# Optimization experiments

Hardware: AMD Instinct MI355X
Metric: run time of the kernel (lower is better)

## Reference

```python
import jax, jax.numpy as jnp
import numpy as np

B, C, L = 4, 256, 4096
H = 8
DK = C // H


def setup_inputs() -> dict:
    key = jax.random.key(0)
    kx, kq, kk, kv, kl = jax.random.split(key, 5)
    scale = 1.0 / np.sqrt(C)
    return {
        "x": jax.random.normal(kx, (B, C, L), dtype=jnp.float32),
        "Wq": jax.random.normal(kq, (C, C), dtype=jnp.float32) * scale,
        "Wk": jax.random.normal(kk, (C, C), dtype=jnp.float32) * scale,
        "Wv": jax.random.normal(kv, (C, C), dtype=jnp.float32) * scale,
        "Wl": jax.random.normal(kl, (C, C), dtype=jnp.float32) * scale,
    }


def reference(x, Wq, Wk, Wv, Wl):
    # Conv1d with kernel_size=1, no bias == channel-mixing matmul per position.
    def proj(W, t):  # W: [C_out, C_in], t: [B, C_in, L] -> [B, L, H, DK]
        y = jnp.einsum('oc,bcl->blo', W, t)
        return y.reshape(B, L, H, DK)

    q = proj(Wq, x)  # [B, L, H, DK]
    k = proj(Wk, x)
    v = proj(Wv, x)

    # scores: [B, H, L, L]
    scores = jnp.einsum('bqhd,bkhd->bhqk', q, k) / jnp.sqrt(jnp.float32(DK))
    p_attn = jax.nn.softmax(scores, axis=-1)
    # attention output with post-ReLU: [B, L, H, DK] -> [B, L, C]
    out = jax.nn.relu(jnp.einsum('bhqk,bkhd->bqhd', p_attn, v)).reshape(B, L, C)
    # last_conv: [B, C_out, L]
    return jnp.einsum('oc,blc->bol', Wl, out)
```

## Files before the change

kernel.cpp:

```cpp
#include <hip/hip_runtime.h>

#define L_DIM 4096
#define C_DIM 256
#define B_DIM 4
#define NH 8
#define DK 32

#define QSCALE 0.25507694f

typedef __bf16 bf16x8 __attribute__((ext_vector_type(8)));
typedef float  f32x4  __attribute__((ext_vector_type(4)));
typedef float  f32x8  __attribute__((ext_vector_type(8)));
typedef float  f32x16 __attribute__((ext_vector_type(16)));

static __device__ __forceinline__ unsigned pk_bf16(float lo, float hi) {
    unsigned a = __builtin_bit_cast(unsigned, lo) + 0x8000u;
    unsigned b = __builtin_bit_cast(unsigned, hi) + 0x8000u;
    return __builtin_amdgcn_perm(b, a, 0x07060302u);
}

__global__ __launch_bounds__(256) void transpose_x_kernel(
    const float* __restrict__ x, __bf16* __restrict__ xt)
{
    const int t  = threadIdx.x;
    const int l0 = blockIdx.x * 64;
    const int c0 = blockIdx.y * 64;
    const int b  = blockIdx.z;

    __shared__ __attribute__((aligned(16))) float T[64][65];

    {
        const int r  = t >> 2;
        const int lc = (t & 3) * 16;
        const float* xp = x + ((size_t)b * C_DIM + c0 + r) * L_DIM + l0 + lc;
        #pragma unroll
        for (int k = 0; k < 4; ++k)
            *(f32x4*)&T[r][lc + k * 4] = *(const f32x4*)(xp + k * 4);
    }
    __syncthreads();
    {
        const int l  = t >> 2;
        const int cc = (t & 3) * 16;
        unsigned u[8];
        #pragma unroll
        for (int i = 0; i < 8; ++i)
            u[i] = pk_bf16(T[cc + 2 * i][l], T[cc + 2 * i + 1][l]);
        __bf16* op = xt + ((size_t)b * L_DIM + l0 + l) * C_DIM + c0 + cc;
        *(uint4*)op       = make_uint4(u[0], u[1], u[2], u[3]);
        *(uint4*)(op + 8) = make_uint4(u[4], u[5], u[6], u[7]);
    }
}

__global__ __launch_bounds__(256) void proj_mfma_kernel(
    const __bf16* __restrict__ xt, const float* __restrict__ Wq,
    const float* __restrict__ Wk, const float* __restrict__ Wv,
    __bf16* __restrict__ Qb, __bf16* __restrict__ Kb, __bf16* __restrict__ Vb)
{
    const int t    = threadIdx.x;
    const int wave = t >> 6;
    const int lane = t & 63;
    const int n32  = lane & 31;
    const int hl   = lane >> 5;
    const int l0   = blockIdx.x * 128;
    const int ob   = blockIdx.y & 1;
    const int p    = blockIdx.y >> 1;
    const int b    = blockIdx.z;
    const float* W = (p == 0) ? Wq : ((p == 1) ? Wk : Wv);
    const float sc = (p == 0) ? QSCALE : 1.0f;

    __shared__ __attribute__((aligned(16))) __bf16 Wt[128][72];
    __shared__ __attribute__((aligned(16))) __bf16 Xs[128][72];

    const int wo  = t >> 1, wcc = (t & 1) * 32;
    const int xl  = t >> 1, xcc = (t & 1) * 32;
    const float*  wg = W + (size_t)(ob * 128 + wo) * C_DIM + wcc;
    const __bf16* xg = xt + ((size_t)b * L_DIM + l0 + xl) * C_DIM + xcc;

    const int moff = (wave & 1) * 64;
    const int noff = (wave >> 1) * 64;

    f32x16 acc[2][2];
    #pragma unroll
    for (int i = 0; i < 2; ++i)
        #pragma unroll
        for (int j = 0; j < 2; ++j)
            #pragma unroll
            for (int r = 0; r < 16; ++r) acc[i][j][r] = 0.f;

    unsigned wpk[16];
    bf16x8   xpr[4];
    #pragma unroll
    for (int k = 0; k < 8; ++k) {
        f32x4 wv = *(const f32x4*)(wg + k * 4);
        wpk[k * 2]     = pk_bf16(wv[0] * sc, wv[1] * sc);
        wpk[k * 2 + 1] = pk_bf16(wv[2] * sc, wv[3] * sc);
    }
    #pragma unroll
    for (int g = 0; g < 4; ++g) xpr[g] = *(const bf16x8*)(xg + g * 8);

    for (int bk = 0; bk < 4; ++bk) {
        __syncthreads();
        #pragma unroll
        for (int g = 0; g < 4; ++g) {
            *(uint4*)&Wt[wo][wcc + g * 8] =
                make_uint4(wpk[g*4], wpk[g*4+1], wpk[g*4+2], wpk[g*4+3]);
            *(bf16x8*)&Xs[xl][xcc + g * 8] = xpr[g];
        }
        if (bk < 3) {
            #pragma unroll
            for (int k = 0; k < 8; ++k) {
                f32x4 wv = *(const f32x4*)(wg + (bk + 1) * 64 + k * 4);
                wpk[k * 2]     = pk_bf16(wv[0] * sc, wv[1] * sc);
                wpk[k * 2 + 1] = pk_bf16(wv[2] * sc, wv[3] * sc);
            }
            #pragma unroll
            for (int g = 0; g < 4; ++g)
                xpr[g] = *(const bf16x8*)(xg + (bk + 1) * 64 + g * 8);
        }
        __syncthreads();

        #pragma unroll
        for (int ks = 0; ks < 4; ++ks) {
            bf16x8 a0 = *(const bf16x8*)&Wt[moff + n32     ][ks * 16 + hl * 8];
            bf16x8 a1 = *(const bf16x8*)&Wt[moff + 32 + n32][ks * 16 + hl * 8];
            bf16x8 b0 = *(const bf16x8*)&Xs[noff + n32     ][ks * 16 + hl * 8];
            bf16x8 b1 = *(const bf16x8*)&Xs[noff + 32 + n32][ks * 16 + hl * 8];
            acc[0][0] = __builtin_amdgcn_mfma_f32_32x32x16_bf16(a0, b0, acc[0][0], 0, 0, 0);
            acc[0][1] = __builtin_amdgcn_mfma_f32_32x32x16_bf16(a0, b1, acc[0][1], 0, 0, 0);
            acc[1][0] = __builtin_amdgcn_mfma_f32_32x32x16_bf16(a1, b0, acc[1][0], 0, 0, 0);
            acc[1][1] = __builtin_amdgcn_mfma_f32_32x32x16_bf16(a1, b1, acc[1][1], 0, 0, 0);
        }
    }

    #pragma unroll
    for (int mt = 0; mt < 2; ++mt) {
        const int o32 = ob * 128 + moff + mt * 32;
        const int h   = o32 >> 5;
        const int bh  = b * NH + h;
        #pragma unroll
        for (int nt = 0; nt < 2; ++nt) {
            const int l = l0 + noff + nt * 32 + n32;
            if (p < 2) {
                __bf16* out = ((p == 0) ? Qb : Kb) + ((size_t)bh * L_DIM + l) * DK;
                #pragma unroll
                for (int g = 0; g < 4; ++g) {
                    unsigned u0 = pk_bf16(acc[mt][nt][g*4],     acc[mt][nt][g*4+1]);
                    unsigned u1 = pk_bf16(acc[mt][nt][g*4+2],   acc[mt][nt][g*4+3]);
                    *(uint2*)(out + 4 * hl + 8 * g) = make_uint2(u0, u1);
                }
            } else {
                #pragma unroll
                for (int r = 0; r < 16; ++r) {
                    const int dk = (r & 3) + 4 * hl + 8 * (r >> 2);
                    Vb[((size_t)bh * DK + dk) * L_DIM + l] = (__bf16)acc[mt][nt][r];
                }
            }
        }
    }
}

__global__ __launch_bounds__(256) void attn_kernel(
    const __bf16* __restrict__ Q, const __bf16* __restrict__ K,
    const __bf16* __restrict__ V, __bf16* __restrict__ Op0,
    __bf16* __restrict__ Op1, float* __restrict__ Ls)
{
    const int tid   = threadIdx.x;
    const int wave  = tid >> 6;
    const int lane  = tid & 63;
    const int n32   = lane & 31;
    const int hl    = lane >> 5;
    const int h     = blockIdx.y;
    const int b     = blockIdx.z >> 1;
    const int khalf = blockIdx.z & 1;
    const int bh    = b * NH + h;
    const int q0    = blockIdx.x * 256 + wave * 64;
    const int kt0   = khalf * 32;

    __shared__ __attribute__((aligned(16))) __bf16 Ks[2][64][40];
    __shared__ __attribute__((aligned(16))) __bf16 Vs[2][32][72];

    bf16x8 qf[2][2];
    #pragma unroll
    for (int qt = 0; qt < 2; ++qt) {
        const __bf16* qp = Q + ((size_t)bh * L_DIM + q0 + qt * 32 + n32) * DK;
        qf[qt][0] = *(const bf16x8*)(qp + hl * 8);
        qf[qt][1] = *(const bf16x8*)(qp + 16 + hl * 8);
    }

    f32x16 oacc[2], lacc[2];
    #pragma unroll
    for (int qt = 0; qt < 2; ++qt)
        #pragma unroll
        for (int r = 0; r < 16; ++r) { oacc[qt][r] = 0.f; lacc[qt][r] = 0.f; }

    const f32x16 z16 = {};

    bf16x8 ones;
    #pragma unroll
    for (int j = 0; j < 8; ++j) ones[j] = (__bf16)1.0f;

    const __bf16* kg = K + (size_t)bh * L_DIM * DK + (tid >> 2) * DK + (tid & 3) * 8;
    const __bf16* vg = V + ((size_t)bh * DK + (tid >> 3)) * L_DIM + (tid & 7) * 8;
    const int kr = tid >> 2, kc = (tid & 3) * 8;
    const int va = tid & 7;
    const int vr = tid >> 3, vc = (va >> 1) * 16 + (va & 1) * 4;

    bf16x8 kreg = *(const bf16x8*)(kg + (size_t)kt0 * 64 * DK);
    bf16x8 vreg = *(const bf16x8*)(vg + kt0 * 64);
    *(bf16x8*)&Ks[0][kr][kc] = kreg;
    {
        union { bf16x8 v; uint2 u2[2]; } vv; vv.v = vreg;
        *(uint2*)&Vs[0][vr][vc]     = vv.u2[0];
        *(uint2*)&Vs[0][vr][vc + 8] = vv.u2[1];
    }
    kreg = *(const bf16x8*)(kg + (size_t)(kt0 + 1) * 64 * DK);
    vreg = *(const bf16x8*)(vg + (kt0 + 1) * 64);

    #pragma unroll 2
    for (int kt = 0; kt < 32; ++kt) {
        const int cur = kt & 1;
        __syncthreads();

        bf16x8 kf[2][2];
        kf[0][0] = *(const bf16x8*)&Ks[cur][n32     ][hl * 8];
        kf[0][1] = *(const bf16x8*)&Ks[cur][n32     ][16 + hl * 8];
        kf[1][0] = *(const bf16x8*)&Ks[cur][32 + n32][hl * 8];
        kf[1][1] = *(const bf16x8*)&Ks[cur][32 + n32][16 + hl * 8];
        bf16x8 vf[4];
        vf[0] = *(const bf16x8*)&Vs[cur][n32][     hl * 8];
        vf[1] = *(const bf16x8*)&Vs[cur][n32][16 + hl * 8];
        vf[2] = *(const bf16x8*)&Vs[cur][n32][32 + hl * 8];
        vf[3] = *(const bf16x8*)&Vs[cur][n32][48 + hl * 8];

        if (kt < 31) {
            *(bf16x8*)&Ks[cur ^ 1][kr][kc] = kreg;
            union { bf16x8 v; uint2 u2[2]; } vv; vv.v = vreg;
            *(uint2*)&Vs[cur ^ 1][vr][vc]     = vv.u2[0];
            *(uint2*)&Vs[cur ^ 1][vr][vc + 8] = vv.u2[1];
            const int nkt = kt0 + ((kt + 2) & 31);
            kreg = *(const bf16x8*)(kg + (size_t)nkt * 64 * DK);
            vreg = *(const bf16x8*)(vg + nkt * 64);
        }

        #pragma unroll
        for (int mt = 0; mt < 2; ++mt) {
            #pragma unroll
            for (int qt = 0; qt < 2; ++qt) {
                f32x16 s = __builtin_amdgcn_mfma_f32_32x32x16_bf16(
                    kf[mt][0], qf[qt][0], z16, 0, 0, 0);
                s = __builtin_amdgcn_mfma_f32_32x32x16_bf16(
                    kf[mt][1], qf[qt][1], s, 0, 0, 0);

                f32x8 e0, e1;
                #pragma unroll
                for (int r = 0; r < 8; ++r) {
                    e0[r] = __builtin_amdgcn_exp2f(s[r]);
                    e1[r] = __builtin_amdgcn_exp2f(s[8 + r]);
                }
                bf16x8 p0 = __builtin_convertvector(e0, bf16x8);
                bf16x8 p1 = __builtin_convertvector(e1, bf16x8);

                oacc[qt] = __builtin_amdgcn_mfma_f32_32x32x16_bf16(
                    vf[mt * 2],     p0, oacc[qt], 0, 0, 0);
                lacc[qt] = __builtin_amdgcn_mfma_f32_32x32x16_bf16(
                    ones,           p0, lacc[qt], 0, 0, 0);
                oacc[qt] = __builtin_amdgcn_mfma_f32_32x32x16_bf16(
                    vf[mt * 2 + 1], p1, oacc[qt], 0, 0, 0);
                lacc[qt] = __builtin_amdgcn_mfma_f32_32x32x16_bf16(
                    ones,           p1, lacc[qt], 0, 0, 0);
            }
        }
    }

    __bf16* Op = khalf ? Op1 : Op0;
    #pragma unroll
    for (int qt = 0; qt < 2; ++qt) {
        const int l = q0 + qt * 32 + n32;
        __bf16* ap = Op + ((size_t)b * L_DIM + l) * C_DIM + h * 32 + 4 * hl;
        #pragma unroll
        for (int g = 0; g < 4; ++g) {
            *(uint2*)(ap + 8 * g) = make_uint2(
                pk_bf16(oacc[qt][g*4],     oacc[qt][g*4+1]),
                pk_bf16(oacc[qt][g*4+2],   oacc[qt][g*4+3]));
        }
        Ls[((size_t)khalf * B_DIM * NH + bh) * L_DIM + l] = lacc[qt][0];
    }
}

__global__ __launch_bounds__(256) void final_mfma_kernel(
    const __bf16* __restrict__ Op0, const __bf16* __restrict__ Op1,
    const float* __restrict__ Ls, const float* __restrict__ Wl,
    float* __restrict__ y)
{
    const int t    = threadIdx.x;
    const int wave = t >> 6;
    const int lane = t & 63;
    const int n32  = lane & 31;
    const int hl   = lane >> 5;
    const int l0   = blockIdx.x * 64;
    const int ob   = blockIdx.y;
    const int b    = blockIdx.z;

    __shared__ __attribute__((aligned(16))) __bf16 Wt[128][72];
    __shared__ __attribute__((aligned(16))) __bf16 Xs[64][72];

    const int wo  = t >> 1, wcc = (t & 1) * 32;
    const int xl  = t >> 2, xcc = (t & 3) * 16;
    const float* wg = Wl + (size_t)(ob * 128 + wo) * C_DIM + wcc;
    const size_t obase = ((size_t)b * L_DIM + l0 + xl) * C_DIM + xcc;

    float inv[4];
    {
        const int lidx = l0 + xl;
        #pragma unroll
        for (int bk = 0; bk < 4; ++bk) {
            const int hh = (bk * 64 + xcc) >> 5;
            const float l1 = Ls[((size_t)0 * B_DIM * NH + b * NH + hh) * L_DIM + lidx];
            const float l2 = Ls[((size_t)1 * B_DIM * NH + b * NH + hh) * L_DIM + lidx];
            inv[bk] = __builtin_amdgcn_rcpf(l1 + l2);
        }
    }

    const int moff = (wave & 1) * 64;
    const int noff = (wave >> 1) * 32;

    f32x16 acc[2];
    #pragma unroll
    for (int i = 0; i < 2; ++i)
        #pragma unroll
        for (int r = 0; r < 16; ++r) acc[i][r] = 0.f;

    unsigned wpk[16];
    bf16x8   o1r, o2r;
    #pragma unroll
    for (int k = 0; k < 8; ++k) {
        f32x4 wv = *(const f32x4*)(wg + k * 4);
        wpk[k * 2]     = pk_bf16(wv[0], wv[1]);
        wpk[k * 2 + 1] = pk_bf16(wv[2], wv[3]);
    }
    o1r = *(const bf16x8*)(Op0 + obase);
    o2r = *(const bf16x8*)(Op1 + obase);
    bf16x8 o1r2 = *(const bf16x8*)(Op0 + obase + 8);
    bf16x8 o2r2 = *(const bf16x8*)(Op1 + obase + 8);

    for (int bk = 0; bk < 4; ++bk) {
        __syncthreads();
        #pragma unroll
        for (int g = 0; g < 4; ++g)
            *(uint4*)&Wt[wo][wcc + g * 8] =
                make_uint4(wpk[g*4], wpk[g*4+1], wpk[g*4+2], wpk[g*4+3]);
        {
            unsigned u[4];
            #pragma unroll
            for (int i = 0; i < 4; ++i) {
                float v0 = ((float)o1r[2*i]   + (float)o2r[2*i]  ) * inv[bk];
                float v1 = ((float)o1r[2*i+1] + (float)o2r[2*i+1]) * inv[bk];
                v0 = v0 > 0.f ? v0 : 0.f;
                v1 = v1 > 0.f ? v1 : 0.f;
                u[i] = pk_bf16(v0, v1);
            }
            *(uint4*)&Xs[xl][xcc] = make_uint4(u[0], u[1], u[2], u[3]);
            #pragma unroll
            for (int i = 0; i < 4; ++i) {
                float v0 = ((float)o1r2[2*i]   + (float)o2r2[2*i]  ) * inv[bk];
                float v1 = ((float)o1r2[2*i+1] + (float)o2r2[2*i+1]) * inv[bk];
                v0 = v0 > 0.f ? v0 : 0.f;
                v1 = v1 > 0.f ? v1 : 0.f;
                u[i] = pk_bf16(v0, v1);
            }
            *(uint4*)&Xs[xl][xcc + 8] = make_uint4(u[0], u[1], u[2], u[3]);
        }
        if (bk < 3) {
            #pragma unroll
            for (int k = 0; k < 8; ++k) {
                f32x4 wv = *(const f32x4*)(wg + (bk + 1) * 64 + k * 4);
                wpk[k * 2]     = pk_bf16(wv[0], wv[1]);
                wpk[k * 2 + 1] = pk_bf16(wv[2], wv[3]);
            }
            o1r  = *(const bf16x8*)(Op0 + obase + (bk + 1) * 64);
            o2r  = *(const bf16x8*)(Op1 + obase + (bk + 1) * 64);
            o1r2 = *(const bf16x8*)(Op0 + obase + (bk + 1) * 64 + 8);
            o2r2 = *(const bf16x8*)(Op1 + obase + (bk + 1) * 64 + 8);
        }
        __syncthreads();

        #pragma unroll
        for (int ks = 0; ks < 4; ++ks) {
            bf16x8 a0 = *(const bf16x8*)&Wt[moff + n32     ][ks * 16 + hl * 8];
            bf16x8 a1 = *(const bf16x8*)&Wt[moff + 32 + n32][ks * 16 + hl * 8];
            bf16x8 b0 = *(const bf16x8*)&Xs[noff + n32     ][ks * 16 + hl * 8];
            acc[0] = __builtin_amdgcn_mfma_f32_32x32x16_bf16(a0, b0, acc[0], 0, 0, 0);
            acc[1] = __builtin_amdgcn_mfma_f32_32x32x16_bf16(a1, b0, acc[1], 0, 0, 0);
        }
    }

    #pragma unroll
    for (int mt = 0; mt < 2; ++mt) {
        #pragma unroll
        for (int r = 0; r < 16; ++r) {
            const int o = ob * 128 + moff + mt * 32 + (r & 3) + 4 * hl + 8 * (r >> 2);
            y[((size_t)b * C_DIM + o) * L_DIM + l0 + noff + n32] = acc[mt][r];
        }
    }
}

extern "C" void kernel_launch(void* const* d_in, const int* in_sizes, int n_in,
                              void* d_out, int out_size, void* d_ws, size_t ws_size,
                              hipStream_t stream)
{
    const float* x  = (const float*)d_in[0];
    const float* Wq = (const float*)d_in[1];
    const float* Wk = (const float*)d_in[2];
    const float* Wv = (const float*)d_in[3];
    const float* Wl = (const float*)d_in[4];
    float* y = (float*)d_out;

    const size_t n = (size_t)B_DIM * NH * L_DIM * DK;
    __bf16* Qb  = (__bf16*)d_ws;
    __bf16* Kb  = Qb + n;
    __bf16* Vb  = Kb + n;
    __bf16* Xt  = Vb + n;
    __bf16* Op0 = Xt;
    __bf16* Op1 = Xt + n;
    float*  Ls  = (float*)(Op1 + n);

    transpose_x_kernel<<<dim3(L_DIM/64, C_DIM/64, B_DIM), 256, 0, stream>>>(x, Xt);
    proj_mfma_kernel<<<dim3(L_DIM/128, 6, B_DIM), 256, 0, stream>>>(
        Xt, Wq, Wk, Wv, Qb, Kb, Vb);
    attn_kernel<<<dim3(L_DIM/256, NH, B_DIM * 2), 256, 0, stream>>>(
        Qb, Kb, Vb, Op0, Op1, Ls);
    final_mfma_kernel<<<dim3(L_DIM/64, 2, B_DIM), 256, 0, stream>>>(
        Op0, Op1, Ls, Wl, y);
}
```

Measured before the change: 211.2 us.

## Double attention K/V tile to 128 keys and interleave LDS fragment loads

The attention kernel now stages 128 keys per iteration instead of 64, so it runs 16 loop iterations with half as many barriers. Each thread loads two 16-byte chunks of K and V per stage. K/V fragments are read from LDS inside the mt loop right before they are used, not all up front, which lowers register pressure. s_setprio raises wave priority around the MFMA/exp section. LDS use roughly doubles, which could cut occupancy, and the new V shared-memory permutation must still match the MFMA operand layout.

Result: no change. 211.2 us (-0.0%).

```diff
diff --git a/kernel.cpp b/kernel.cpp
--- a/kernel.cpp
+++ b/kernel.cpp
@@ -165,19 +165,18 @@
     __bf16* __restrict__ Op1, float* __restrict__ Ls)
 {
     const int tid   = threadIdx.x;
-    const int wave  = tid >> 6;
     const int lane  = tid & 63;
     const int n32   = lane & 31;
     const int hl    = lane >> 5;
+    const int wave  = tid >> 6;
     const int h     = blockIdx.y;
     const int b     = blockIdx.z >> 1;
     const int khalf = blockIdx.z & 1;
     const int bh    = b * NH + h;
     const int q0    = blockIdx.x * 256 + wave * 64;
-    const int kt0   = khalf * 32;
-
-    __shared__ __attribute__((aligned(16))) __bf16 Ks[2][64][40];
-    __shared__ __attribute__((aligned(16))) __bf16 Vs[2][32][72];
+
+    __shared__ __attribute__((aligned(16))) __bf16 Ks[2][128][40];
+    __shared__ __attribute__((aligned(16))) __bf16 Vs[2][32][136];
 
     bf16x8 qf[2][2];
     #pragma unroll
@@ -199,57 +198,67 @@
     #pragma unroll
     for (int j = 0; j < 8; ++j) ones[j] = (__bf16)1.0f;
 
-    const __bf16* kg = K + (size_t)bh * L_DIM * DK + (tid >> 2) * DK + (tid & 3) * 8;
-    const __bf16* vg = V + ((size_t)bh * DK + (tid >> 3)) * L_DIM + (tid & 7) * 8;
-    const int kr = tid >> 2, kc = (tid & 3) * 8;
-    const int va = tid & 7;
-    const int vr = tid >> 3, vc = (va >> 1) * 16 + (va & 1) * 4;
-
-    bf16x8 kreg = *(const bf16x8*)(kg + (size_t)kt0 * 64 * DK);
-    bf16x8 vreg = *(const bf16x8*)(vg + kt0 * 64);
-    *(bf16x8*)&Ks[0][kr][kc] = kreg;
+    const __bf16* kg = K + (size_t)bh * L_DIM * DK + (size_t)khalf * 2048 * DK
+                         + (tid >> 1) * DK + (tid & 1) * 16;
+    const __bf16* vg = V + ((size_t)bh * DK + (tid >> 3)) * L_DIM
+                         + khalf * 2048 + (tid & 7) * 16;
+    const int kr = tid >> 1, kc = (tid & 1) * 16;
+    const int j16 = (tid & 7) * 16;
+    const int vr  = tid >> 3;
+
+    bf16x8 kreg0 = *(const bf16x8*)(kg);
+    bf16x8 kreg1 = *(const bf16x8*)(kg + 8);
+    bf16x8 vreg0 = *(const bf16x8*)(vg);
+    bf16x8 vreg1 = *(const bf16x8*)(vg + 8);
     {
-        union { bf16x8 v; uint2 u2[2]; } vv; vv.v = vreg;
-        *(uint2*)&Vs[0][vr][vc]     = vv.u2[0];
-        *(uint2*)&Vs[0][vr][vc + 8] = vv.u2[1];
-    }
-    kreg = *(const bf16x8*)(kg + (size_t)(kt0 + 1) * 64 * DK);
-    vreg = *(const bf16x8*)(vg + (kt0 + 1) * 64);
+        *(bf16x8*)&Ks[0][kr][kc]     = kreg0;
+        *(bf16x8*)&Ks[0][kr][kc + 8] = kreg1;
+        union { bf16x8 v; uint2 u2[2]; } v0, v1;
+        v0.v = vreg0; v1.v = vreg1;
+        *(uint2*)&Vs[0][vr][j16]      = v0.u2[0];
+        *(uint2*)&Vs[0][vr][j16 + 8]  = v0.u2[1];
+        *(uint2*)&Vs[0][vr][j16 + 4]  = v1.u2[0];
+        *(uint2*)&Vs[0][vr][j16 + 12] = v1.u2[1];
+    }
+    kreg0 = *(const bf16x8*)(kg + (size_t)1 * 128 * DK);
+    kreg1 = *(const bf16x8*)(kg + (size_t)1 * 128 * DK + 8);
+    vreg0 = *(const bf16x8*)(vg + 128);
+    vreg1 = *(const bf16x8*)(vg + 128 + 8);
 
     #pragma unroll 2
-    for (int kt = 0; kt < 32; ++kt) {
+    for (int kt = 0; kt < 16; ++kt) {
         const int cur = kt & 1;
         __syncthreads();
 
-        bf16x8 kf[2][2];
-        kf[0][0] = *(const bf16x8*)&Ks[cur][n32     ][hl * 8];
-        kf[0][1] = *(const bf16x8*)&Ks[cur][n32     ][16 + hl * 8];
-        kf[1][0] = *(const bf16x8*)&Ks[cur][32 + n32][hl * 8];
-        kf[1][1] = *(const bf16x8*)&Ks[cur][32 + n32][16 + hl * 8];
-        bf16x8 vf[4];
-        vf[0] = *(const bf16x8*)&Vs[cur][n32][     hl * 8];
-        vf[1] = *(const bf16x8*)&Vs[cur][n32][16 + hl * 8];
-        vf[2] = *(const bf16x8*)&Vs[cur][n32][32 + hl * 8];
-        vf[3] = *(const bf16x8*)&Vs[cur][n32][48 + hl * 8];
-
-        if (kt < 31) {
-            *(bf16x8*)&Ks[cur ^ 1][kr][kc] = kreg;
-            union { bf16x8 v; uint2 u2[2]; } vv; vv.v = vreg;
-            *(uint2*)&Vs[cur ^ 1][vr][vc]     = vv.u2[0];
-            *(uint2*)&Vs[cur ^ 1][vr][vc + 8] = vv.u2[1];
-            const int nkt = kt0 + ((kt + 2) & 31);
-            kreg = *(const bf16x8*)(kg + (size_t)nkt * 64 * DK);
-            vreg = *(const bf16x8*)(vg + nkt * 64);
-        }
-
-        #pragma unroll
-        for (int mt = 0; mt < 2; ++mt) {
+        if (kt < 15) {
+            *(bf16x8*)&Ks[cur ^ 1][kr][kc]     = kreg0;
+            *(bf16x8*)&Ks[cur ^ 1][kr][kc + 8] = kreg1;
+            union { bf16x8 v; uint2 u2[2]; } v0, v1;
+            v0.v = vreg0; v1.v = vreg1;
+            *(uint2*)&Vs[cur ^ 1][vr][j16]      = v0.u2[0];
+            *(uint2*)&Vs[cur ^ 1][vr][j16 + 8]  = v0.u2[1];
+            *(uint2*)&Vs[cur ^ 1][vr][j16 + 4]  = v1.u2[0];
+            *(uint2*)&Vs[cur ^ 1][vr][j16 + 12] = v1.u2[1];
+            const int nkt = (kt + 2) & 15;
+            kreg0 = *(const bf16x8*)(kg + (size_t)nkt * 128 * DK);
+            kreg1 = *(const bf16x8*)(kg + (size_t)nkt * 128 * DK + 8);
+            vreg0 = *(const bf16x8*)(vg + nkt * 128);
+            vreg1 = *(const bf16x8*)(vg + nkt * 128 + 8);
+        }
+
+        __builtin_amdgcn_s_setprio(1);
+        #pragma unroll
+        for (int mt = 0; mt < 4; ++mt) {
+            bf16x8 kf0 = *(const bf16x8*)&Ks[cur][mt * 32 + n32][hl * 8];
+            bf16x8 kf1 = *(const bf16x8*)&Ks[cur][mt * 32 + n32][16 + hl * 8];
+            bf16x8 vfA = *(const bf16x8*)&Vs[cur][n32][mt * 32 + hl * 8];
+            bf16x8 vfB = *(const bf16x8*)&Vs[cur][n32][mt * 32 + 16 + hl * 8];
             #pragma unroll
             for (int qt = 0; qt < 2; ++qt) {
                 f32x16 s = __builtin_amdgcn_mfma_f32_32x32x16_bf16(
-                    kf[mt][0], qf[qt][0], z16, 0, 0, 0);
+                    kf0, qf[qt][0], z16, 0, 0, 0);
                 s = __builtin_amdgcn_mfma_f32_32x32x16_bf16(
-                    kf[mt][1], qf[qt][1], s, 0, 0, 0);
+                    kf1, qf[qt][1], s, 0, 0, 0);
 
                 f32x8 e0, e1;
                 #pragma unroll
@@ -261,15 +270,16 @@
                 bf16x8 p1 = __builtin_convertvector(e1, bf16x8);
 
                 oacc[qt] = __builtin_amdgcn_mfma_f32_32x32x16_bf16(
-                    vf[mt * 2],     p0, oacc[qt], 0, 0, 0);
+                    vfA,  p0, oacc[qt], 0, 0, 0);
                 lacc[qt] = __builtin_amdgcn_mfma_f32_32x32x16_bf16(
-                    ones,           p0, lacc[qt], 0, 0, 0);
+                    ones, p0, lacc[qt], 0, 0, 0);
                 oacc[qt] = __builtin_amdgcn_mfma_f32_32x32x16_bf16(
-                    vf[mt * 2 + 1], p1, oacc[qt], 0, 0, 0);
+                    vfB,  p1, oacc[qt], 0, 0, 0);
                 lacc[qt] = __builtin_amdgcn_mfma_f32_32x32x16_bf16(
-                    ones,           p1, lacc[qt], 0, 0, 0);
-            }
-        }
+                    ones, p1, lacc[qt], 0, 0, 0);
+            }
+        }
+        __builtin_amdgcn_s_setprio(0);
     }
 
     __bf16* Op = khalf ? Op1 : Op0;
```
